# Kernel tuning notes

Hardware: AMD Instinct MI355X
Metric: run time of the kernel (lower is better)

Reference implementation:

```python
import jax, jax.numpy as jnp
import numpy as np

TAU = 0.1      # Gumbel-Sinkhorn temperature (module default)
N_ITER = 100   # Sinkhorn iterations (module default)
B, N = 16, 256


def setup_inputs() -> dict:
    key = jax.random.key(0)
    alpha = jax.random.normal(key, (B, N, N), dtype=jnp.float32)
    return {"alpha": alpha}


def _log_sinkhorn(log_alpha, n_iter):
    # Successive row / column normalization in log space.
    # Note: the torch original early-exits once the column sums are within
    # eps=1e-6 of 1; once converged, further iterations are (numerically)
    # identity, so a fixed n_iter loop computes the same result. We use a
    # fixed-length lax.scan, which runs the whole loop on-device with no
    # per-step host sync.
    def step(la, _):
        la = la - jax.nn.logsumexp(la, axis=-1, keepdims=True)  # row normalize
        la = la - jax.nn.logsumexp(la, axis=-2, keepdims=True)  # col normalize
        return la, None

    log_alpha, _ = jax.lax.scan(step, log_alpha, None, length=n_iter)
    return jnp.exp(log_alpha)


def reference(alpha):
    # Training path of GumbelSinkhornPermutation.forward:
    # scale by temperature, then Sinkhorn-normalize to a near doubly-stochastic
    # matrix. (wandb logging side effects omitted.)
    return _log_sinkhorn(alpha / TAU, N_ITER)
```

## Files before the change

kernel.cpp:

```cpp
#include <hip/hip_runtime.h>

#define N_ITER 100

typedef float f32x4 __attribute__((ext_vector_type(4)));
typedef unsigned u32x4 __attribute__((ext_vector_type(4)));

__device__ __forceinline__ unsigned bf16pack(float a, float b) {
  unsigned ua = __float_as_uint(a), ub = __float_as_uint(b);
  ua = (ua + 0x7FFFu + ((ua >> 16) & 1u)) >> 16;
  ub = (ub + 0x7FFFu + ((ub >> 16) & 1u)) >> 16;
  return ua | (ub << 16);
}
__device__ __forceinline__ float bflo(unsigned u) { return __uint_as_float(u << 16); }
__device__ __forceinline__ float bfhi(unsigned u) { return __uint_as_float(u & 0xFFFF0000u); }

__device__ __forceinline__ void pin_agpr(u32x4& x) {
  asm("" : "=a"(x) : "0"(x));
}

__device__ __forceinline__ void mfma_first(f32x4& acc, const u32x4& a, const u32x4& b) {
  asm("s_nop 2\n\tv_mfma_f32_16x16x32_bf16 %0, %1, %2, 0"
      : "=&a"(acc) : "a"(a), "v"(b));
}
__device__ __forceinline__ void mfma_aa(f32x4& acc, const u32x4& a, const u32x4& b) {
  asm("v_mfma_f32_16x16x32_bf16 %0, %1, %2, %0"
      : "+a"(acc) : "a"(a), "v"(b));
}
__device__ __forceinline__ void mfma_fence(f32x4& acc0, f32x4& acc1) {
  asm volatile("s_nop 7\n\ts_nop 7\n\ts_nop 7" : "+a"(acc0), "+a"(acc1));
}

__global__ __launch_bounds__(512)
__attribute__((amdgpu_waves_per_eu(2, 2)))
void sinkhorn_mfma8f(const float* __restrict__ alpha, float* __restrict__ out) {
  __shared__ alignas(16) unsigned short Cb16[256];
  __shared__ alignas(16) unsigned short Rb16[256];
  __shared__ alignas(16) float Cb32[256];
  __shared__ alignas(16) float Rb32[256];

  const int tid  = threadIdx.x;
  const int lane = tid & 63;
  const int w    = tid >> 6;
  const int m    = lane & 15;
  const int q    = lane >> 4;

  const size_t mbase = (size_t)blockIdx.x * (256 * 256);
  const float* A = alpha + mbase;
  float*       O = out + mbase;

  u32x4 arow[2][8];
  u32x4 acol[2][8];

#pragma unroll
  for (int s = 0; s < 2; ++s) {
    const float* rowp = A + (size_t)(32 * w + 16 * s + m) * 256 + 8 * q;
#pragma unroll
    for (int c = 0; c < 8; ++c) {
      float4 x0 = *(const float4*)(rowp + 32 * c);
      float4 x1 = *(const float4*)(rowp + 32 * c + 4);
      arow[s][c] = (u32x4){bf16pack(__expf(x0.x * 10.0f), __expf(x0.y * 10.0f)),
                           bf16pack(__expf(x0.z * 10.0f), __expf(x0.w * 10.0f)),
                           bf16pack(__expf(x1.x * 10.0f), __expf(x1.y * 10.0f)),
                           bf16pack(__expf(x1.z * 10.0f), __expf(x1.w * 10.0f))};
    }
    const float* colp = A + (size_t)(8 * q) * 256 + 32 * w + 16 * s + m;
#pragma unroll
    for (int c = 0; c < 8; ++c) {
      const float* p = colp + (size_t)(32 * c) * 256;
      acol[s][c] =
          (u32x4){bf16pack(__expf(p[0] * 10.0f), __expf(p[256] * 10.0f)),
                  bf16pack(__expf(p[512] * 10.0f), __expf(p[768] * 10.0f)),
                  bf16pack(__expf(p[1024] * 10.0f), __expf(p[1280] * 10.0f)),
                  bf16pack(__expf(p[1536] * 10.0f), __expf(p[1792] * 10.0f))};
    }
  }
#pragma unroll
  for (int s = 0; s < 2; ++s)
#pragma unroll
    for (int c = 0; c < 8; ++c) {
      pin_agpr(arow[s][c]);
      pin_agpr(acol[s][c]);
    }

  if (tid < 256) Cb16[tid] = 0x3F80;
  __syncthreads();

  for (int it = 0; it < N_ITER; ++it) {
    const bool last = (it == N_ITER - 1);

    {
      u32x4 B[8];
#pragma unroll
      for (int c = 0; c < 8; ++c) B[c] = *(const u32x4*)&Cb16[32 * c + 8 * q];
      f32x4 acc0, acc1;
      mfma_first(acc0, arow[0][0], B[0]);
      mfma_first(acc1, arow[1][0], B[0]);
#pragma unroll
      for (int c = 1; c < 8; ++c) {
        mfma_aa(acc0, arow[0][c], B[c]);
        mfma_aa(acc1, arow[1][c], B[c]);
      }
      mfma_fence(acc0, acc1);
      if (m == 0) {
        float r0 = __builtin_amdgcn_rcpf(acc0[0]);
        float r1 = __builtin_amdgcn_rcpf(acc0[1]);
        float r2 = __builtin_amdgcn_rcpf(acc0[2]);
        float r3 = __builtin_amdgcn_rcpf(acc0[3]);
        float r4 = __builtin_amdgcn_rcpf(acc1[0]);
        float r5 = __builtin_amdgcn_rcpf(acc1[1]);
        float r6 = __builtin_amdgcn_rcpf(acc1[2]);
        float r7 = __builtin_amdgcn_rcpf(acc1[3]);
        *(uint2*)&Rb16[32 * w + 4 * q] = make_uint2(bf16pack(r0, r1), bf16pack(r2, r3));
        *(uint2*)&Rb16[32 * w + 16 + 4 * q] = make_uint2(bf16pack(r4, r5), bf16pack(r6, r7));
        if (last) {
          *(float4*)&Rb32[32 * w + 4 * q] = make_float4(r0, r1, r2, r3);
          *(float4*)&Rb32[32 * w + 16 + 4 * q] = make_float4(r4, r5, r6, r7);
        }
      }
    }
    __syncthreads();

    {
      u32x4 B[8];
#pragma unroll
      for (int c = 0; c < 8; ++c) B[c] = *(const u32x4*)&Rb16[32 * c + 8 * q];
      f32x4 acc0, acc1;
      mfma_first(acc0, acol[0][0], B[0]);
      mfma_first(acc1, acol[1][0], B[0]);
#pragma unroll
      for (int c = 1; c < 8; ++c) {
        mfma_aa(acc0, acol[0][c], B[c]);
        mfma_aa(acc1, acol[1][c], B[c]);
      }
      mfma_fence(acc0, acc1);
      if (m == 0) {
        float c0 = __builtin_amdgcn_rcpf(acc0[0]);
        float c1 = __builtin_amdgcn_rcpf(acc0[1]);
        float c2 = __builtin_amdgcn_rcpf(acc0[2]);
        float c3 = __builtin_amdgcn_rcpf(acc0[3]);
        float c4 = __builtin_amdgcn_rcpf(acc1[0]);
        float c5 = __builtin_amdgcn_rcpf(acc1[1]);
        float c6 = __builtin_amdgcn_rcpf(acc1[2]);
        float c7 = __builtin_amdgcn_rcpf(acc1[3]);
        *(uint2*)&Cb16[32 * w + 4 * q] = make_uint2(bf16pack(c0, c1), bf16pack(c2, c3));
        *(uint2*)&Cb16[32 * w + 16 + 4 * q] = make_uint2(bf16pack(c4, c5), bf16pack(c6, c7));
        if (last) {
          *(float4*)&Cb32[32 * w + 4 * q] = make_float4(c0, c1, c2, c3);
          *(float4*)&Cb32[32 * w + 16 + 4 * q] = make_float4(c4, c5, c6, c7);
        }
      }
    }
    __syncthreads();
  }

#pragma unroll
  for (int s = 0; s < 2; ++s) {
    const float Rm = Rb32[32 * w + 16 * s + m];
    float* dst = O + (size_t)(32 * w + 16 * s + m) * 256 + 8 * q;
#pragma unroll
    for (int c = 0; c < 8; ++c) {
      float4 c0 = *(const float4*)&Cb32[32 * c + 8 * q];
      float4 c1 = *(const float4*)&Cb32[32 * c + 8 * q + 4];
      u32x4 pk = arow[s][c];
      float4 o0, o1;
      o0.x = bflo(pk.x) * Rm * c0.x;
      o0.y = bfhi(pk.x) * Rm * c0.y;
      o0.z = bflo(pk.y) * Rm * c0.z;
      o0.w = bfhi(pk.y) * Rm * c0.w;
      o1.x = bflo(pk.z) * Rm * c1.x;
      o1.y = bfhi(pk.z) * Rm * c1.y;
      o1.z = bflo(pk.w) * Rm * c1.z;
      o1.w = bfhi(pk.w) * Rm * c1.w;
      *(float4*)(dst + 32 * c) = o0;
      *(float4*)(dst + 32 * c + 4) = o1;
    }
  }
}

extern "C" void kernel_launch(void* const* d_in, const int* in_sizes, int n_in,
                              void* d_out, int out_size, void* d_ws, size_t ws_size,
                              hipStream_t stream) {
  const float* alpha = (const float*)d_in[0];
  float* out = (float*)d_out;
  sinkhorn_mfma8f<<<dim3(16), dim3(512), 0, stream>>>(alpha, out);
}
```

Baseline: 169.2 us.

## Use four waves per matrix with four MFMA chains each and VGPR accumulators

Halves the block from 8 to 4 waves per 256x256 matrix, so each wave holds 64 rows and 64 columns of the exp'd bf16 matrix in AGPRs and runs four interleaved MFMA accumulation chains instead of two. Accumulators move from AGPRs to VGPRs, and only the first MFMA keeps its leading nop. The reciprocal writeback is spread across four lanes using selects rather than done by one lane. The aim is to cut barrier cost and hide MFMA latency with more independent chains, at the cost of longer per-wave MFMA sequences and much higher register pressure per wave.

```diff
diff --git a/kernel.cpp b/kernel.cpp
--- a/kernel.cpp
+++ b/kernel.cpp
@@ -18,21 +18,26 @@
   asm("" : "=a"(x) : "0"(x));
 }
 
+__device__ __forceinline__ void mfma_first_nop(f32x4& acc, const u32x4& a, const u32x4& b) {
+  asm("s_nop 2\n\tv_mfma_f32_16x16x32_bf16 %0, %1, %2, 0"
+      : "=&v"(acc) : "a"(a), "v"(b));
+}
 __device__ __forceinline__ void mfma_first(f32x4& acc, const u32x4& a, const u32x4& b) {
-  asm("s_nop 2\n\tv_mfma_f32_16x16x32_bf16 %0, %1, %2, 0"
-      : "=&a"(acc) : "a"(a), "v"(b));
+  asm("v_mfma_f32_16x16x32_bf16 %0, %1, %2, 0"
+      : "=&v"(acc) : "a"(a), "v"(b));
 }
 __device__ __forceinline__ void mfma_aa(f32x4& acc, const u32x4& a, const u32x4& b) {
   asm("v_mfma_f32_16x16x32_bf16 %0, %1, %2, %0"
-      : "+a"(acc) : "a"(a), "v"(b));
+      : "+v"(acc) : "a"(a), "v"(b));
 }
-__device__ __forceinline__ void mfma_fence(f32x4& acc0, f32x4& acc1) {
-  asm volatile("s_nop 7\n\ts_nop 7\n\ts_nop 7" : "+a"(acc0), "+a"(acc1));
+__device__ __forceinline__ void mfma_fence4(f32x4& a0, f32x4& a1, f32x4& a2, f32x4& a3) {
+  asm volatile("s_nop 7\n\ts_nop 7\n\ts_nop 7"
+               : "+v"(a0), "+v"(a1), "+v"(a2), "+v"(a3));
 }
 
-__global__ __launch_bounds__(512)
-__attribute__((amdgpu_waves_per_eu(2, 2)))
-void sinkhorn_mfma8f(const float* __restrict__ alpha, float* __restrict__ out) {
+__global__ __launch_bounds__(256)
+__attribute__((amdgpu_waves_per_eu(1, 1)))
+void sinkhorn_mfma4w(const float* __restrict__ alpha, float* __restrict__ out) {
   __shared__ alignas(16) unsigned short Cb16[256];
   __shared__ alignas(16) unsigned short Rb16[256];
   __shared__ alignas(16) float Cb32[256];
@@ -48,12 +53,12 @@
   const float* A = alpha + mbase;
   float*       O = out + mbase;
 
-  u32x4 arow[2][8];
-  u32x4 acol[2][8];
+  u32x4 arow[4][8];
+  u32x4 acol[4][8];
 
 #pragma unroll
-  for (int s = 0; s < 2; ++s) {
-    const float* rowp = A + (size_t)(32 * w + 16 * s + m) * 256 + 8 * q;
+  for (int s = 0; s < 4; ++s) {
+    const float* rowp = A + (size_t)(64 * w + 16 * s + m) * 256 + 8 * q;
 #pragma unroll
     for (int c = 0; c < 8; ++c) {
       float4 x0 = *(const float4*)(rowp + 32 * c);
@@ -62,8 +67,9 @@
                            bf16pack(__expf(x0.z * 10.0f), __expf(x0.w * 10.0f)),
                            bf16pack(__expf(x1.x * 10.0f), __expf(x1.y * 10.0f)),
                            bf16pack(__expf(x1.z * 10.0f), __expf(x1.w * 10.0f))};
+      pin_agpr(arow[s][c]);
     }
-    const float* colp = A + (size_t)(8 * q) * 256 + 32 * w + 16 * s + m;
+    const float* colp = A + (size_t)(8 * q) * 256 + 64 * w + 16 * s + m;
 #pragma unroll
     for (int c = 0; c < 8; ++c) {
       const float* p = colp + (size_t)(32 * c) * 256;
@@ -72,17 +78,11 @@
                   bf16pack(__expf(p[512] * 10.0f), __expf(p[768] * 10.0f)),
                   bf16pack(__expf(p[1024] * 10.0f), __expf(p[1280] * 10.0f)),
                   bf16pack(__expf(p[1536] * 10.0f), __expf(p[1792] * 10.0f))};
+      pin_agpr(acol[s][c]);
     }
   }
-#pragma unroll
-  for (int s = 0; s < 2; ++s)
-#pragma unroll
-    for (int c = 0; c < 8; ++c) {
-      pin_agpr(arow[s][c]);
-      pin_agpr(acol[s][c]);
-    }
 
-  if (tid < 256) Cb16[tid] = 0x3F80;
+  Cb16[tid] = 0x3F80;
   __syncthreads();
 
   for (int it = 0; it < N_ITER; ++it) {
@@ -92,30 +92,31 @@
       u32x4 B[8];
 #pragma unroll
       for (int c = 0; c < 8; ++c) B[c] = *(const u32x4*)&Cb16[32 * c + 8 * q];
-      f32x4 acc0, acc1;
-      mfma_first(acc0, arow[0][0], B[0]);
+      f32x4 acc0, acc1, acc2, acc3;
+      mfma_first_nop(acc0, arow[0][0], B[0]);
       mfma_first(acc1, arow[1][0], B[0]);
+      mfma_first(acc2, arow[2][0], B[0]);
+      mfma_first(acc3, arow[3][0], B[0]);
 #pragma unroll
       for (int c = 1; c < 8; ++c) {
         mfma_aa(acc0, arow[0][c], B[c]);
         mfma_aa(acc1, arow[1][c], B[c]);
+        mfma_aa(acc2, arow[2][c], B[c]);
+        mfma_aa(acc3, arow[3][c], B[c]);
       }
-      mfma_fence(acc0, acc1);
-      if (m == 0) {
-        float r0 = __builtin_amdgcn_rcpf(acc0[0]);
-        float r1 = __builtin_amdgcn_rcpf(acc0[1]);
-        float r2 = __builtin_amdgcn_rcpf(acc0[2]);
-        float r3 = __builtin_amdgcn_rcpf(acc0[3]);
-        float r4 = __builtin_amdgcn_rcpf(acc1[0]);
-        float r5 = __builtin_amdgcn_rcpf(acc1[1]);
-        float r6 = __builtin_amdgcn_rcpf(acc1[2]);
-        float r7 = __builtin_amdgcn_rcpf(acc1[3]);
-        *(uint2*)&Rb16[32 * w + 4 * q] = make_uint2(bf16pack(r0, r1), bf16pack(r2, r3));
-        *(uint2*)&Rb16[32 * w + 16 + 4 * q] = make_uint2(bf16pack(r4, r5), bf16pack(r6, r7));
-        if (last) {
-          *(float4*)&Rb32[32 * w + 4 * q] = make_float4(r0, r1, r2, r3);
-          *(float4*)&Rb32[32 * w + 16 + 4 * q] = make_float4(r4, r5, r6, r7);
-        }
+      mfma_fence4(acc0, acc1, acc2, acc3);
+      if (m < 4) {
+        f32x4 sA = (m & 1) ? acc1 : acc0;
+        f32x4 sB = (m & 1) ? acc3 : acc2;
+        f32x4 sv = (m & 2) ? sB : sA;
+        float r0 = __builtin_amdgcn_rcpf(sv[0]);
+        float r1 = __builtin_amdgcn_rcpf(sv[1]);
+        float r2 = __builtin_amdgcn_rcpf(sv[2]);
+        float r3 = __builtin_amdgcn_rcpf(sv[3]);
+        *(uint2*)&Rb16[64 * w + 16 * m + 4 * q] =
+            make_uint2(bf16pack(r0, r1), bf16pack(r2, r3));
+        if (last)
+          *(float4*)&Rb32[64 * w + 16 * m + 4 * q] = make_float4(r0, r1, r2, r3);
       }
     }
     __syncthreads();
@@ -124,39 +125,40 @@
       u32x4 B[8];
 #pragma unroll
       for (int c = 0; c < 8; ++c) B[c] = *(const u32x4*)&Rb16[32 * c + 8 * q];
-      f32x4 acc0, acc1;
-      mfma_first(acc0, acol[0][0], B[0]);
+      f32x4 acc0, acc1, acc2, acc3;
+      mfma_first_nop(acc0, acol[0][0], B[0]);
       mfma_first(acc1, acol[1][0], B[0]);
+      mfma_first(acc2, acol[2][0], B[0]);
+      mfma_first(acc3, acol[3][0], B[0]);
 #pragma unroll
       for (int c = 1; c < 8; ++c) {
         mfma_aa(acc0, acol[0][c], B[c]);
         mfma_aa(acc1, acol[1][c], B[c]);
+        mfma_aa(acc2, acol[2][c], B[c]);
+        mfma_aa(acc3, acol[3][c], B[c]);
       }
-      mfma_fence(acc0, acc1);
-      if (m == 0) {
-        float c0 = __builtin_amdgcn_rcpf(acc0[0]);
-        float c1 = __builtin_amdgcn_rcpf(acc0[1]);
-        float c2 = __builtin_amdgcn_rcpf(acc0[2]);
-        float c3 = __builtin_amdgcn_rcpf(acc0[3]);
-        float c4 = __builtin_amdgcn_rcpf(acc1[0]);
-        float c5 = __builtin_amdgcn_rcpf(acc1[1]);
-        float c6 = __builtin_amdgcn_rcpf(acc1[2]);
-        float c7 = __builtin_amdgcn_rcpf(acc1[3]);
-        *(uint2*)&Cb16[32 * w + 4 * q] = make_uint2(bf16pack(c0, c1), bf16pack(c2, c3));
-        *(uint2*)&Cb16[32 * w + 16 + 4 * q] = make_uint2(bf16pack(c4, c5), bf16pack(c6, c7));
-        if (last) {
-          *(float4*)&Cb32[32 * w + 4 * q] = make_float4(c0, c1, c2, c3);
-          *(float4*)&Cb32[32 * w + 16 + 4 * q] = make_float4(c4, c5, c6, c7);
-        }
+      mfma_fence4(acc0, acc1, acc2, acc3);
+      if (m < 4) {
+        f32x4 sA = (m & 1) ? acc1 : acc0;
+        f32x4 sB = (m & 1) ? acc3 : acc2;
+        f32x4 sv = (m & 2) ? sB : sA;
+        float c0 = __builtin_amdgcn_rcpf(sv[0]);
+        float c1 = __builtin_amdgcn_rcpf(sv[1]);
+        float c2 = __builtin_amdgcn_rcpf(sv[2]);
+        float c3 = __builtin_amdgcn_rcpf(sv[3]);
+        *(uint2*)&Cb16[64 * w + 16 * m + 4 * q] =
+            make_uint2(bf16pack(c0, c1), bf16pack(c2, c3));
+        if (last)
+          *(float4*)&Cb32[64 * w + 16 * m + 4 * q] = make_float4(c0, c1, c2, c3);
       }
     }
     __syncthreads();
   }
 
 #pragma unroll
-  for (int s = 0; s < 2; ++s) {
-    const float Rm = Rb32[32 * w + 16 * s + m];
-    float* dst = O + (size_t)(32 * w + 16 * s + m) * 256 + 8 * q;
+  for (int s = 0; s < 4; ++s) {
+    const float Rm = Rb32[64 * w + 16 * s + m];
+    float* dst = O + (size_t)(64 * w + 16 * s + m) * 256 + 8 * q;
 #pragma unroll
     for (int c = 0; c < 8; ++c) {
       float4 c0 = *(const float4*)&Cb32[32 * c + 8 * q];
@@ -182,5 +184,5 @@
                               hipStream_t stream) {
   const float* alpha = (const float*)d_in[0];
   float* out = (float*)d_out;
-  sinkhorn_mfma8f<<<dim3(16), dim3(512), 0, stream>>>(alpha, out);
+  sinkhorn_mfma4w<<<dim3(16), dim3(256), 0, stream>>>(alpha, out);
 }
```

Result: slower. 174.9 us (+3.3%).

## Exit the Sinkhorn loop early once bf16 row/column scalings reach a fixed point

Applied to the files above, without the earlier changes.

Every lane now computes the packed bf16 reciprocals and compares them with the previous row and column scaling vectors held in shared memory. Each wave votes on whether all its values are unchanged and records the vote in a shared flag byte. When all eight waves agree, the loop breaks. Because iterations are deterministic, an unchanged state would repeat exactly, so skipping the rest should not change the result. The final full-precision row/column pass is peeled out of the loop. This adds extra LDS reads, comparisons and a wave vote to every iteration, and it only saves time if the bf16 state actually stops changing well before the iteration limit.

```diff
diff --git a/kernel.cpp b/kernel.cpp
--- a/kernel.cpp
+++ b/kernel.cpp
@@ -32,11 +32,12 @@
 
 __global__ __launch_bounds__(512)
 __attribute__((amdgpu_waves_per_eu(2, 2)))
-void sinkhorn_mfma8f(const float* __restrict__ alpha, float* __restrict__ out) {
+void sinkhorn_mfma8c(const float* __restrict__ alpha, float* __restrict__ out) {
   __shared__ alignas(16) unsigned short Cb16[256];
   __shared__ alignas(16) unsigned short Rb16[256];
   __shared__ alignas(16) float Cb32[256];
   __shared__ alignas(16) float Rb32[256];
+  __shared__ alignas(8) unsigned Fl[2];
 
   const int tid  = threadIdx.x;
   const int lane = tid & 63;
@@ -82,16 +83,26 @@
       pin_agpr(acol[s][c]);
     }
 
-  if (tid < 256) Cb16[tid] = 0x3F80;
+  if (tid < 256) {
+    Cb16[tid] = 0x3F80;
+    Rb16[tid] = 0;
+  }
+  if (tid < 2) Fl[tid] = 0;
   __syncthreads();
 
-  for (int it = 0; it < N_ITER; ++it) {
-    const bool last = (it == N_ITER - 1);
+  for (int it = 0; it < N_ITER - 1; ++it) {
+    {
+      uint2 fl = *(const uint2*)Fl;
+      if (fl.x == 0x01010101u && fl.y == 0x01010101u) break;
+    }
+    bool rsame = true, csame = true;
 
     {
       u32x4 B[8];
 #pragma unroll
       for (int c = 0; c < 8; ++c) B[c] = *(const u32x4*)&Cb16[32 * c + 8 * q];
+      uint2 oldR0 = *(const uint2*)&Rb16[32 * w + 4 * q];
+      uint2 oldR1 = *(const uint2*)&Rb16[32 * w + 16 + 4 * q];
       f32x4 acc0, acc1;
       mfma_first(acc0, arow[0][0], B[0]);
       mfma_first(acc1, arow[1][0], B[0]);
@@ -101,21 +112,20 @@
         mfma_aa(acc1, arow[1][c], B[c]);
       }
       mfma_fence(acc0, acc1);
+      float r0 = __builtin_amdgcn_rcpf(acc0[0]);
+      float r1 = __builtin_amdgcn_rcpf(acc0[1]);
+      float r2 = __builtin_amdgcn_rcpf(acc0[2]);
+      float r3 = __builtin_amdgcn_rcpf(acc0[3]);
+      float r4 = __builtin_amdgcn_rcpf(acc1[0]);
+      float r5 = __builtin_amdgcn_rcpf(acc1[1]);
+      float r6 = __builtin_amdgcn_rcpf(acc1[2]);
+      float r7 = __builtin_amdgcn_rcpf(acc1[3]);
+      unsigned u0 = bf16pack(r0, r1), u1 = bf16pack(r2, r3);
+      unsigned u2 = bf16pack(r4, r5), u3 = bf16pack(r6, r7);
+      rsame = (u0 == oldR0.x) & (u1 == oldR0.y) & (u2 == oldR1.x) & (u3 == oldR1.y);
       if (m == 0) {
-        float r0 = __builtin_amdgcn_rcpf(acc0[0]);
-        float r1 = __builtin_amdgcn_rcpf(acc0[1]);
-        float r2 = __builtin_amdgcn_rcpf(acc0[2]);
-        float r3 = __builtin_amdgcn_rcpf(acc0[3]);
-        float r4 = __builtin_amdgcn_rcpf(acc1[0]);
-        float r5 = __builtin_amdgcn_rcpf(acc1[1]);
-        float r6 = __builtin_amdgcn_rcpf(acc1[2]);
-        float r7 = __builtin_amdgcn_rcpf(acc1[3]);
-        *(uint2*)&Rb16[32 * w + 4 * q] = make_uint2(bf16pack(r0, r1), bf16pack(r2, r3));
-        *(uint2*)&Rb16[32 * w + 16 + 4 * q] = make_uint2(bf16pack(r4, r5), bf16pack(r6, r7));
-        if (last) {
-          *(float4*)&Rb32[32 * w + 4 * q] = make_float4(r0, r1, r2, r3);
-          *(float4*)&Rb32[32 * w + 16 + 4 * q] = make_float4(r4, r5, r6, r7);
-        }
+        *(uint2*)&Rb16[32 * w + 4 * q] = make_uint2(u0, u1);
+        *(uint2*)&Rb16[32 * w + 16 + 4 * q] = make_uint2(u2, u3);
       }
     }
     __syncthreads();
@@ -124,6 +134,8 @@
       u32x4 B[8];
 #pragma unroll
       for (int c = 0; c < 8; ++c) B[c] = *(const u32x4*)&Rb16[32 * c + 8 * q];
+      uint2 oldC0 = *(const uint2*)&Cb16[32 * w + 4 * q];
+      uint2 oldC1 = *(const uint2*)&Cb16[32 * w + 16 + 4 * q];
       f32x4 acc0, acc1;
       mfma_first(acc0, acol[0][0], B[0]);
       mfma_first(acc1, acol[1][0], B[0]);
@@ -133,25 +145,83 @@
         mfma_aa(acc1, acol[1][c], B[c]);
       }
       mfma_fence(acc0, acc1);
+      float c0 = __builtin_amdgcn_rcpf(acc0[0]);
+      float c1 = __builtin_amdgcn_rcpf(acc0[1]);
+      float c2 = __builtin_amdgcn_rcpf(acc0[2]);
+      float c3 = __builtin_amdgcn_rcpf(acc0[3]);
+      float c4 = __builtin_amdgcn_rcpf(acc1[0]);
+      float c5 = __builtin_amdgcn_rcpf(acc1[1]);
+      float c6 = __builtin_amdgcn_rcpf(acc1[2]);
+      float c7 = __builtin_amdgcn_rcpf(acc1[3]);
+      unsigned u0 = bf16pack(c0, c1), u1 = bf16pack(c2, c3);
+      unsigned u2 = bf16pack(c4, c5), u3 = bf16pack(c6, c7);
+      csame = (u0 == oldC0.x) & (u1 == oldC0.y) & (u2 == oldC1.x) & (u3 == oldC1.y);
       if (m == 0) {
-        float c0 = __builtin_amdgcn_rcpf(acc0[0]);
-        float c1 = __builtin_amdgcn_rcpf(acc0[1]);
-        float c2 = __builtin_amdgcn_rcpf(acc0[2]);
-        float c3 = __builtin_amdgcn_rcpf(acc0[3]);
-        float c4 = __builtin_amdgcn_rcpf(acc1[0]);
-        float c5 = __builtin_amdgcn_rcpf(acc1[1]);
-        float c6 = __builtin_amdgcn_rcpf(acc1[2]);
-        float c7 = __builtin_amdgcn_rcpf(acc1[3]);
-        *(uint2*)&Cb16[32 * w + 4 * q] = make_uint2(bf16pack(c0, c1), bf16pack(c2, c3));
-        *(uint2*)&Cb16[32 * w + 16 + 4 * q] = make_uint2(bf16pack(c4, c5), bf16pack(c6, c7));
-        if (last) {
-          *(float4*)&Cb32[32 * w + 4 * q] = make_float4(c0, c1, c2, c3);
-          *(float4*)&Cb32[32 * w + 16 + 4 * q] = make_float4(c4, c5, c6, c7);
-        }
-      }
+        *(uint2*)&Cb16[32 * w + 4 * q] = make_uint2(u0, u1);
+        *(uint2*)&Cb16[32 * w + 16 + 4 * q] = make_uint2(u2, u3);
+      }
+      bool wconv = __all(rsame & csame) != 0;
+      if (lane == 0) ((unsigned char*)Fl)[w] = wconv ? 1 : 0;
     }
     __syncthreads();
   }
+
+  {
+    u32x4 B[8];
+#pragma unroll
+    for (int c = 0; c < 8; ++c) B[c] = *(const u32x4*)&Cb16[32 * c + 8 * q];
+    f32x4 acc0, acc1;
+    mfma_first(acc0, arow[0][0], B[0]);
+    mfma_first(acc1, arow[1][0], B[0]);
+#pragma unroll
+    for (int c = 1; c < 8; ++c) {
+      mfma_aa(acc0, arow[0][c], B[c]);
+      mfma_aa(acc1, arow[1][c], B[c]);
+    }
+    mfma_fence(acc0, acc1);
+    if (m == 0) {
+      float r0 = __builtin_amdgcn_rcpf(acc0[0]);
+      float r1 = __builtin_amdgcn_rcpf(acc0[1]);
+      float r2 = __builtin_amdgcn_rcpf(acc0[2]);
+      float r3 = __builtin_amdgcn_rcpf(acc0[3]);
+      float r4 = __builtin_amdgcn_rcpf(acc1[0]);
+      float r5 = __builtin_amdgcn_rcpf(acc1[1]);
+      float r6 = __builtin_amdgcn_rcpf(acc1[2]);
+      float r7 = __builtin_amdgcn_rcpf(acc1[3]);
+      *(uint2*)&Rb16[32 * w + 4 * q] = make_uint2(bf16pack(r0, r1), bf16pack(r2, r3));
+      *(uint2*)&Rb16[32 * w + 16 + 4 * q] = make_uint2(bf16pack(r4, r5), bf16pack(r6, r7));
+      *(float4*)&Rb32[32 * w + 4 * q] = make_float4(r0, r1, r2, r3);
+      *(float4*)&Rb32[32 * w + 16 + 4 * q] = make_float4(r4, r5, r6, r7);
+    }
+  }
+  __syncthreads();
+  {
+    u32x4 B[8];
+#pragma unroll
+    for (int c = 0; c < 8; ++c) B[c] = *(const u32x4*)&Rb16[32 * c + 8 * q];
+    f32x4 acc0, acc1;
+    mfma_first(acc0, acol[0][0], B[0]);
+    mfma_first(acc1, acol[1][0], B[0]);
+#pragma unroll
+    for (int c = 1; c < 8; ++c) {
+      mfma_aa(acc0, acol[0][c], B[c]);
+      mfma_aa(acc1, acol[1][c], B[c]);
+    }
+    mfma_fence(acc0, acc1);
+    if (m == 0) {
+      float c0 = __builtin_amdgcn_rcpf(acc0[0]);
+      float c1 = __builtin_amdgcn_rcpf(acc0[1]);
+      float c2 = __builtin_amdgcn_rcpf(acc0[2]);
+      float c3 = __builtin_amdgcn_rcpf(acc0[3]);
+      float c4 = __builtin_amdgcn_rcpf(acc1[0]);
+      float c5 = __builtin_amdgcn_rcpf(acc1[1]);
+      float c6 = __builtin_amdgcn_rcpf(acc1[2]);
+      float c7 = __builtin_amdgcn_rcpf(acc1[3]);
+      *(float4*)&Cb32[32 * w + 4 * q] = make_float4(c0, c1, c2, c3);
+      *(float4*)&Cb32[32 * w + 16 + 4 * q] = make_float4(c4, c5, c6, c7);
+    }
+  }
+  __syncthreads();
 
 #pragma unroll
   for (int s = 0; s < 2; ++s) {
@@ -182,5 +252,5 @@
                               hipStream_t stream) {
   const float* alpha = (const float*)d_in[0];
   float* out = (float*)d_out;
-  sinkhorn_mfma8f<<<dim3(16), dim3(512), 0, stream>>>(alpha, out);
-}
+  sinkhorn_mfma8c<<<dim3(16), dim3(512), 0, stream>>>(alpha, out);
+}
```

After: 187.5 us. +10.8%, slower.
